# Performance work log

Measured on AMD Instinct MI355X. Metric: run time of the kernel, lower is better.

## Reference

```python
import jax, jax.numpy as jnp
import numpy as np

B, S, H, NH = 1, 4096, 1024, 16
HD = H // NH  # 64


def _rope_tables(seq_len, dim):
    inv_freq = 1.0 / (10000.0 ** (np.arange(0, dim, 2, dtype=np.float32) / dim))
    t = np.arange(seq_len, dtype=np.float32)
    freqs = np.outer(t, inv_freq)                 # [S, dim/2]
    emb = np.concatenate([freqs, freqs], axis=-1)  # [S, dim]
    return jnp.asarray(np.cos(emb)), jnp.asarray(np.sin(emb))


def setup_inputs() -> dict:
    key = jax.random.key(0)
    ks = jax.random.split(key, 5)
    hidden_states = jax.random.normal(ks[0], (B, S, H), dtype=jnp.float32)
    scale = 1.0 / np.sqrt(H)
    Wq = jax.random.normal(ks[1], (H, H), dtype=jnp.float32) * scale
    Wk = jax.random.normal(ks[2], (H, H), dtype=jnp.float32) * scale
    Wv = jax.random.normal(ks[3], (H, H), dtype=jnp.float32) * scale
    Wo = jax.random.normal(ks[4], (H, H), dtype=jnp.float32) * scale
    cos, sin = _rope_tables(S, HD)
    # additive causal mask [1,1,S,S]
    causal = jnp.where(
        jnp.tril(jnp.ones((S, S), dtype=bool)), 0.0, jnp.float32(-1e9)
    )[None, None]
    return {
        "hidden_states": hidden_states,
        "cos": cos,
        "sin": sin,
        "attention_mask": causal,
        "Wq": Wq,
        "Wk": Wk,
        "Wv": Wv,
        "Wo": Wo,
    }


def _rotate_half(x):
    x1, x2 = jnp.split(x, 2, axis=-1)
    return jnp.concatenate([-x2, x1], axis=-1)


def _apply_rope(q, k, cos, sin):
    # q,k: [B,NH,S,HD]; cos/sin: [S,HD] -> broadcast [1,1,S,HD]
    cos = cos[None, None]
    sin = sin[None, None]
    q = q * cos + _rotate_half(q) * sin
    k = k * cos + _rotate_half(k) * sin
    return q, k


def reference(hidden_states, cos, sin, attention_mask, Wq, Wk, Wv, Wo):
    bsz, q_len, _ = hidden_states.shape
    q = hidden_states @ Wq.T
    k = hidden_states @ Wk.T
    v = hidden_states @ Wv.T
    # [B,S,H] -> [B,NH,S,HD]
    def split_heads(x):
        return x.reshape(bsz, q_len, NH, HD).transpose(0, 2, 1, 3)
    q, k, v = split_heads(q), split_heads(k), split_heads(v)
    q, k = _apply_rope(q, k, cos, sin)
    scores = jnp.einsum("bhqd,bhkd->bhqk", q, k) / jnp.sqrt(jnp.float32(HD))
    scores = scores + attention_mask
    attn = jax.nn.softmax(scores, axis=-1)
    out = jnp.einsum("bhqk,bhkd->bhqd", attn, v)
    out = out.transpose(0, 2, 1, 3).reshape(bsz, q_len, H)
    return out @ Wo.T
```

## Files before the change

kernel.cpp:

```cpp
#include <hip/hip_runtime.h>

#define S_LEN 4096
#define NHEADS 16
#define HD 64
#define HDIM 1024

typedef __attribute__((ext_vector_type(8))) __bf16 bf16x8;
typedef __attribute__((ext_vector_type(4))) float f32x4;
typedef __attribute__((ext_vector_type(4))) int i32x4;
typedef unsigned short u16;

static __device__ __forceinline__ u16 f2bu(float f) {
    unsigned u = __builtin_bit_cast(unsigned, f);
    u += 0x7FFFu + ((u >> 16) & 1u);
    return (u16)(u >> 16);
}
static __device__ __forceinline__ int pack_bf16(float lo, float hi) {
    return (int)__builtin_amdgcn_perm(__builtin_bit_cast(unsigned, hi),
                                      __builtin_bit_cast(unsigned, lo), 0x07060302u);
}
static __device__ __forceinline__ float fexp2(float x) {
    return __builtin_amdgcn_exp2f(x);
}

static __device__ __forceinline__ bf16x8 read_frag(const u16* lds, int row, int kbyte) {
    int c = kbyte ^ ((row & 7) << 4);
    return *reinterpret_cast<const bf16x8*>(reinterpret_cast<const char*>(lds) + row * 128 + c);
}
static __device__ __forceinline__ bf16x8 read_off(const u16* lds, int byteoff) {
    return *reinterpret_cast<const bf16x8*>(reinterpret_cast<const char*>(lds) + byteoff);
}

static __device__ __forceinline__ void stage_gll(const u16* __restrict__ src, const u16* lds, unsigned ldsbyte) {
    __builtin_amdgcn_global_load_lds(
        (const __attribute__((address_space(1))) void*)src,
        (__attribute__((address_space(3))) void*)(reinterpret_cast<const char*>(lds) + ldsbyte),
        16, 0, 0);
}

static __device__ __forceinline__ void softmax_gather(
    const f32x4* sf, float& l_part, bf16x8* pf, int lj, int lc)
{
    int pk[4][2];
#pragma unroll
    for (int nf = 0; nf < 4; ++nf) {
        float p0 = fexp2(sf[nf][0]);
        float p1 = fexp2(sf[nf][1]);
        float p2 = fexp2(sf[nf][2]);
        float p3 = fexp2(sf[nf][3]);
        l_part += (p0 + p1) + (p2 + p3);
        pk[nf][0] = pack_bf16(p0, p1);
        pk[nf][1] = pack_bf16(p2, p3);
    }
#pragma unroll
    for (int kb = 0; kb < 2; ++kb) {
        i32x4 u;
#pragma unroll
        for (int s = 0; s < 4; ++s) {
            int srcl = lc + (((2 * lj + (s >> 1)) & 3) << 4);
            int v0 = __shfl(pk[2 * kb][s & 1], srcl);
            int v1 = __shfl(pk[2 * kb + 1][s & 1], srcl);
            u[s] = (lj & 2) ? v1 : v0;
        }
        pf[kb] = __builtin_bit_cast(bf16x8, u);
    }
}

__global__ __launch_bounds__(256) void cvt_all(
    const float* __restrict__ X, const float* __restrict__ Wq, const float* __restrict__ Wk,
    const float* __restrict__ Wv, const float* __restrict__ Wo,
    u16* __restrict__ Xb, u16* __restrict__ Wqb, u16* __restrict__ Wkb,
    u16* __restrict__ Wvb, u16* __restrict__ Wob)
{
    int i = blockIdx.x * 256 + threadIdx.x;
    const float* src; u16* dst; int off;
    if (i < (1 << 20)) { src = X; dst = Xb; off = i; }
    else {
        int j = i - (1 << 20);
        int w = j >> 18; off = j & 0x3FFFF;
        src = (w == 0) ? Wq : (w == 1) ? Wk : (w == 2) ? Wv : Wo;
        dst = (w == 0) ? Wqb : (w == 1) ? Wkb : (w == 2) ? Wvb : Wob;
    }
    float4 v = reinterpret_cast<const float4*>(src)[off];
    ushort4 o;
    o.x = f2bu(v.x); o.y = f2bu(v.y); o.z = f2bu(v.z); o.w = f2bu(v.w);
    reinterpret_cast<ushort4*>(dst)[off] = o;
}

__global__ __launch_bounds__(256) void qkv_gemm(
    const u16* __restrict__ A,
    const u16* __restrict__ Wq, const u16* __restrict__ Wk, const u16* __restrict__ Wv,
    u16* __restrict__ Qb, u16* __restrict__ Kb, u16* __restrict__ VTb,
    const float* __restrict__ cosT, const float* __restrict__ sinT)
{
    __shared__ u16 At[128 * 64];
    __shared__ u16 Bt[128 * 64];
    const int z = blockIdx.z;
    const u16* W = (z == 0) ? Wq : (z == 1) ? Wk : Wv;
    const int tid = threadIdx.x;
    const int wid = tid >> 6, lane = tid & 63;
    const int wm = wid >> 1, wn = wid & 1;
    const int lj = lane >> 4, lc = lane & 15;
    const int m0 = blockIdx.x * 128, n0 = blockIdx.y * 128;

    f32x4 acc[4][4];
#pragma unroll
    for (int i = 0; i < 4; ++i)
#pragma unroll
        for (int j = 0; j < 4; ++j) acc[i][j] = 0.0f;

    for (int k0 = 0; k0 < HDIM; k0 += 64) {
        __syncthreads();
#pragma unroll
        for (int r = 0; r < 4; ++r) {
            int idx = (r << 8) + tid;
            int row = idx >> 3;
            int c = (idx & 7) << 4;
            int csw = c ^ ((row & 7) << 4);
            unsigned lb = (unsigned)(idx & ~63) << 4;
            stage_gll(A + (size_t)(m0 + row) * HDIM + k0 + (csw >> 1), At, lb);
            stage_gll(W + (size_t)(n0 + row) * HDIM + k0 + (csw >> 1), Bt, lb);
        }
        __syncthreads();
#pragma unroll
        for (int kb = 0; kb < 2; ++kb) {
            int kbyte = (kb << 6) + (lj << 4);
            bf16x8 af[4], bfr[4];
#pragma unroll
            for (int mf = 0; mf < 4; ++mf) af[mf] = read_frag(At, (wm << 6) + (mf << 4) + lc, kbyte);
#pragma unroll
            for (int nf = 0; nf < 4; ++nf) bfr[nf] = read_frag(Bt, (wn << 6) + (nf << 4) + lc, kbyte);
#pragma unroll
            for (int mf = 0; mf < 4; ++mf)
#pragma unroll
                for (int nf = 0; nf < 4; ++nf)
                    acc[mf][nf] = __builtin_amdgcn_mfma_f32_16x16x32_bf16(af[mf], bfr[nf], acc[mf][nf], 0, 0, 0);
        }
    }

    const int mrow0 = m0 + (wm << 6);
    const int ncol0 = n0 + (wn << 6);
    if (z == 2) {
#pragma unroll
        for (int mf = 0; mf < 4; ++mf)
#pragma unroll
            for (int nf = 0; nf < 4; ++nf)
#pragma unroll
                for (int j = 0; j < 4; ++j) {
                    int s = mrow0 + (mf << 4) + (lj << 2) + j;
                    int o = ncol0 + (nf << 4) + lc;
                    VTb[((size_t)(o >> 6) * HD + (o & 63)) * S_LEN + s] = f2bu(acc[mf][nf][j]);
                }
    } else {
        u16* outB = (z == 0) ? Qb : Kb;
        const float sc = (z == 0) ? 0.18033688011112042f : 1.0f;
#pragma unroll
        for (int mf = 0; mf < 4; ++mf) {
            float nv[4][4];
#pragma unroll
            for (int nf = 0; nf < 4; ++nf)
#pragma unroll
                for (int j = 0; j < 4; ++j) {
                    int s = mrow0 + (mf << 4) + (lj << 2) + j;
                    int o = ncol0 + (nf << 4) + lc;
                    int d = o & 63;
                    float x  = acc[mf][nf][j];
                    float xp = acc[mf][nf ^ 2][j];
                    float cv = cosT[(size_t)s * HD + d];
                    float sv = sinT[(size_t)s * HD + d];
                    float rot = (d < 32) ? -xp : xp;
                    nv[nf][j] = (x * cv + rot * sv) * sc;
                }
#pragma unroll
            for (int nf = 0; nf < 4; ++nf)
#pragma unroll
                for (int j = 0; j < 4; ++j) {
                    int s = mrow0 + (mf << 4) + (lj << 2) + j;
                    int o = ncol0 + (nf << 4) + lc;
                    outB[((size_t)(o >> 6) * S_LEN + s) * HD + (o & 63)] = f2bu(nv[nf][j]);
                }
        }
    }
}

__global__ __launch_bounds__(256) void wo_gemm(
    const u16* __restrict__ A, const u16* __restrict__ W, float* __restrict__ outF)
{
    __shared__ u16 At[128 * 64];
    __shared__ u16 Bt[64 * 64];
    const int tid = threadIdx.x;
    const int wid = tid >> 6, lane = tid & 63;
    const int wm = wid >> 1, wn = wid & 1;
    const int lj = lane >> 4, lc = lane & 15;
    const int m0 = blockIdx.x * 128, n0 = blockIdx.y * 64;

    f32x4 acc[4][2];
#pragma unroll
    for (int i = 0; i < 4; ++i)
#pragma unroll
        for (int j = 0; j < 2; ++j) acc[i][j] = 0.0f;

    for (int k0 = 0; k0 < HDIM; k0 += 64) {
        __syncthreads();
#pragma unroll
        for (int r = 0; r < 4; ++r) {
            int idx = (r << 8) + tid;
            int row = idx >> 3;
            int c = (idx & 7) << 4;
            int csw = c ^ ((row & 7) << 4);
            unsigned lb = (unsigned)(idx & ~63) << 4;
            stage_gll(A + (size_t)(m0 + row) * HDIM + k0 + (csw >> 1), At, lb);
            if (r < 2)
                stage_gll(W + (size_t)(n0 + row) * HDIM + k0 + (csw >> 1), Bt, lb);
        }
        __syncthreads();
#pragma unroll
        for (int kb = 0; kb < 2; ++kb) {
            int kbyte = (kb << 6) + (lj << 4);
            bf16x8 af[4], bfr[2];
#pragma unroll
            for (int mf = 0; mf < 4; ++mf) af[mf] = read_frag(At, (wm << 6) + (mf << 4) + lc, kbyte);
#pragma unroll
            for (int nf = 0; nf < 2; ++nf) bfr[nf] = read_frag(Bt, (wn << 5) + (nf << 4) + lc, kbyte);
#pragma unroll
            for (int mf = 0; mf < 4; ++mf)
#pragma unroll
                for (int nf = 0; nf < 2; ++nf)
                    acc[mf][nf] = __builtin_amdgcn_mfma_f32_16x16x32_bf16(af[mf], bfr[nf], acc[mf][nf], 0, 0, 0);
        }
    }

    const int mrow0 = m0 + (wm << 6);
    const int ncol0 = n0 + (wn << 5);
#pragma unroll
    for (int mf = 0; mf < 4; ++mf)
#pragma unroll
        for (int nf = 0; nf < 2; ++nf)
#pragma unroll
            for (int j = 0; j < 4; ++j) {
                int s = mrow0 + (mf << 4) + (lj << 2) + j;
                int o = ncol0 + (nf << 4) + lc;
                outF[(size_t)s * HDIM + o] = acc[mf][nf][j];
            }
}

__global__ __launch_bounds__(256, 2) void attn_fwd(
    const u16* __restrict__ Q, const u16* __restrict__ K,
    const u16* __restrict__ VT, u16* __restrict__ AO)
{
    __shared__ u16 Kt[2][128 * 64];
    __shared__ u16 Vt[2][2][64 * 64];

    const int tid = threadIdx.x;
    const int wid = tid >> 6, lane = tid & 63;
    const int lj = lane >> 4, lc = lane & 15;

    const int lid = blockIdx.x;
    const int x = lid & 7, g = lid >> 3;
    const int a = g >> 5, c = g & 31;
    const int b = a ? (31 - c) : c;
    const int h = (x << 1) | a;
    const int qtA = 63 - b, qtB = b;
    const int qbaseA = qtA * 64 + wid * 16;
    const int qbaseB = qtB * 64 + wid * 16;
    const int nsteps = qtA + 1;

    const u16* Qh = Q + (size_t)h * S_LEN * HD;

    const int srow = tid >> 3;
    const int csw  = ((tid & 7) << 4) ^ ((srow & 7) << 4);
    const u16* kbase = K  + (size_t)h * S_LEN * HD + (size_t)srow * HD + (csw >> 1);
    const u16* vbase = VT + (size_t)h * HD * S_LEN + (size_t)srow * S_LEN + (csw >> 1);
    const unsigned lb = (unsigned)(tid & ~63) << 4;

#define SK(buf, hf, t) do { \
        const u16* p_ = kbase + (size_t)(t) * 64 * HD; \
        stage_gll(p_,           (const u16*)Kt[buf] + (hf) * 4096, lb); \
        stage_gll(p_ + 32 * HD, (const u16*)Kt[buf] + (hf) * 4096, lb + 4096); \
    } while (0)
#define SV(buf, hf, t) do { \
        const u16* p_ = vbase + (t) * 64; \
        stage_gll(p_,              (const u16*)Vt[buf][hf], lb); \
        stage_gll(p_ + 32 * S_LEN, (const u16*)Vt[buf][hf], lb + 4096); \
    } while (0)

    int foff[2][4];
#pragma unroll
    for (int kb = 0; kb < 2; ++kb)
#pragma unroll
        for (int nf = 0; nf < 4; ++nf) {
            int row = (nf << 4) + lc;
            foff[kb][nf] = row * 128 + (((kb << 6) + (lj << 4)) ^ ((row & 7) << 4));
        }

    bf16x8 qB0[2], qB1[2];
#pragma unroll
    for (int kb = 0; kb < 2; ++kb) {
        qB0[kb] = *reinterpret_cast<const bf16x8*>(
            Qh + (size_t)(qbaseA + lc) * HD + (kb << 5) + (lj << 3));
        qB1[kb] = *reinterpret_cast<const bf16x8*>(
            Qh + (size_t)(qbaseB + lc) * HD + (kb << 5) + (lj << 3));
    }

    f32x4 accO0[4], accO1[4];
    float l0 = 0.0f, l1 = 0.0f;
#pragma unroll
    for (int df = 0; df < 4; ++df) { accO0[df] = 0.0f; accO1[df] = 0.0f; }

    bf16x8 pf0[2], pf1[2], vf[2][4];

    auto compute = [&](int t, const u16* KtH, const u16* VtH) {
        const bool act1 = (t <= qtB);
        const bool pv1  = (t >= 1) && (t <= qtB + 1);

        bf16x8 kf[2][4];
#pragma unroll
        for (int kb = 0; kb < 2; ++kb)
#pragma unroll
            for (int nf = 0; nf < 4; ++nf)
                kf[kb][nf] = read_off(KtH, foff[kb][nf]);

        f32x4 sf0[4], sf1[4];
#pragma unroll
        for (int nf = 0; nf < 4; ++nf) { sf0[nf] = 0.0f; sf1[nf] = 0.0f; }

        __builtin_amdgcn_s_setprio(1);
#pragma unroll
        for (int kb = 0; kb < 2; ++kb)
#pragma unroll
            for (int nf = 0; nf < 4; ++nf)
                sf0[nf] = __builtin_amdgcn_mfma_f32_16x16x32_bf16(kf[kb][nf], qB0[kb], sf0[nf], 0, 0, 0);
        if (act1) {
#pragma unroll
            for (int kb = 0; kb < 2; ++kb)
#pragma unroll
                for (int nf = 0; nf < 4; ++nf)
                    sf1[nf] = __builtin_amdgcn_mfma_f32_16x16x32_bf16(kf[kb][nf], qB1[kb], sf1[nf], 0, 0, 0);
        }
        if (t >= 1) {
#pragma unroll
            for (int kb = 0; kb < 2; ++kb)
#pragma unroll
                for (int df = 0; df < 4; ++df)
                    accO0[df] = __builtin_amdgcn_mfma_f32_16x16x32_bf16(pf0[kb], vf[kb][df], accO0[df], 0, 0, 0);
        }
        if (pv1) {
#pragma unroll
            for (int kb = 0; kb < 2; ++kb)
#pragma unroll
                for (int df = 0; df < 4; ++df)
                    accO1[df] = __builtin_amdgcn_mfma_f32_16x16x32_bf16(pf1[kb], vf[kb][df], accO1[df], 0, 0, 0);
        }
        __builtin_amdgcn_s_setprio(0);

#pragma unroll
        for (int kb = 0; kb < 2; ++kb)
#pragma unroll
            for (int df = 0; df < 4; ++df)
                vf[kb][df] = read_off(VtH, foff[kb][df]);

        const int kv0 = t << 6;
        if (t == qtA) {
            int qg = qbaseA + lc;
#pragma unroll
            for (int nf = 0; nf < 4; ++nf)
#pragma unroll
                for (int j = 0; j < 4; ++j) {
                    int kvg = kv0 + (nf << 4) + (lj << 2) + j;
                    if (kvg > qg) sf0[nf][j] = -1e30f;
                }
        }
        if (act1 && t == qtB) {
            int qg = qbaseB + lc;
#pragma unroll
            for (int nf = 0; nf < 4; ++nf)
#pragma unroll
                for (int j = 0; j < 4; ++j) {
                    int kvg = kv0 + (nf << 4) + (lj << 2) + j;
                    if (kvg > qg) sf1[nf][j] = -1e30f;
                }
        }

        softmax_gather(sf0, l0, pf0, lj, lc);
        if (act1) softmax_gather(sf1, l1, pf1, lj, lc);
    };

    SK(0, 0, 0); SV(0, 0, 0);
    if (nsteps > 1) { SK(0, 1, 1); SV(0, 1, 1); }
    __syncthreads();

    const int nmac = (nsteps + 1) >> 1;
    int cur = 0;
    for (int m = 0; m < nmac; ++m) {
        const int t2 = 2 * m + 2, t3 = 2 * m + 3;
        if (t2 < nsteps) { SK(cur ^ 1, 0, t2); SV(cur ^ 1, 0, t2); }
        if (t3 < nsteps) { SK(cur ^ 1, 1, t3); SV(cur ^ 1, 1, t3); }

        compute(2 * m, (const u16*)Kt[cur], (const u16*)Vt[cur][0]);
        if (2 * m + 1 < nsteps)
            compute(2 * m + 1, (const u16*)Kt[cur] + 4096, (const u16*)Vt[cur][1]);

        __syncthreads();
        cur ^= 1;
    }

#pragma unroll
    for (int kb = 0; kb < 2; ++kb)
#pragma unroll
        for (int df = 0; df < 4; ++df)
            accO0[df] = __builtin_amdgcn_mfma_f32_16x16x32_bf16(pf0[kb], vf[kb][df], accO0[df], 0, 0, 0);

    l0 += __shfl_xor(l0, 16); l0 += __shfl_xor(l0, 32);
    l1 += __shfl_xor(l1, 16); l1 += __shfl_xor(l1, 32);
    float lr0[4], lr1[4];
#pragma unroll
    for (int j = 0; j < 4; ++j) {
        lr0[j] = __shfl(l0, (lj << 2) + j);
        lr1[j] = __shfl(l1, (lj << 2) + j);
    }
#pragma unroll
    for (int df = 0; df < 4; ++df)
#pragma unroll
        for (int j = 0; j < 4; ++j) {
            int sA = qbaseA + (lj << 2) + j;
            int sB = qbaseB + (lj << 2) + j;
            int d = (df << 4) + lc;
            AO[(size_t)sA * HDIM + h * HD + d] = f2bu(accO0[df][j] / lr0[j]);
            AO[(size_t)sB * HDIM + h * HD + d] = f2bu(accO1[df][j] / lr1[j]);
        }
#undef SK
#undef SV
}

extern "C" void kernel_launch(void* const* d_in, const int* in_sizes, int n_in,
                              void* d_out, int out_size, void* d_ws, size_t ws_size,
                              hipStream_t stream) {
    const float* hidden = (const float*)d_in[0];
    const float* cosT   = (const float*)d_in[1];
    const float* sinT   = (const float*)d_in[2];
    const float* Wq = (const float*)d_in[4];
    const float* Wk = (const float*)d_in[5];
    const float* Wv = (const float*)d_in[6];
    const float* Wo = (const float*)d_in[7];
    float* out = (float*)d_out;

    char* ws = (char*)d_ws;
    u16* Xb  = (u16*)(ws);
    u16* Wqb = (u16*)(ws + (size_t)( 8 << 20));
    u16* Wkb = (u16*)(ws + (size_t)(10 << 20));
    u16* Wvb = (u16*)(ws + (size_t)(12 << 20));
    u16* Wob = (u16*)(ws + (size_t)(14 << 20));
    u16* Qb  = (u16*)(ws + (size_t)(16 << 20));
    u16* Kb  = (u16*)(ws + (size_t)(24 << 20));
    u16* VTb = (u16*)(ws + (size_t)(32 << 20));
    u16* AOb = (u16*)(ws + (size_t)(40 << 20));

    cvt_all<<<8192, 256, 0, stream>>>(hidden, Wq, Wk, Wv, Wo, Xb, Wqb, Wkb, Wvb, Wob);

    qkv_gemm<<<dim3(S_LEN / 128, HDIM / 128, 3), 256, 0, stream>>>(
        Xb, Wqb, Wkb, Wvb, Qb, Kb, VTb, cosT, sinT);

    attn_fwd<<<dim3(512), 256, 0, stream>>>(Qb, Kb, VTb, AOb);

    wo_gemm<<<dim3(S_LEN / 128, HDIM / 64), 256, 0, stream>>>(AOb, Wob, out);
}
```

Before: 161.5 us.

## Process paired causal query tiles sequentially instead of sharing KV stream

The attention kernel previously handled two query tiles per block (a long tile and its short complement) in one pass over the KV tiles, reusing each loaded K/V tile for both. It now runs two sequential phases, one per query tile, each with its own KV pipeline. This lowers register pressure and removes the per-step branching for the second tile. In exchange, the K/V tiles for the short tile are loaded from memory a second time.

```diff
diff --git a/kernel.cpp b/kernel.cpp
--- a/kernel.cpp
+++ b/kernel.cpp
@@ -257,13 +257,8 @@
 
     const int lid = blockIdx.x;
     const int x = lid & 7, g = lid >> 3;
-    const int a = g >> 5, c = g & 31;
-    const int b = a ? (31 - c) : c;
-    const int h = (x << 1) | a;
-    const int qtA = 63 - b, qtB = b;
-    const int qbaseA = qtA * 64 + wid * 16;
-    const int qbaseB = qtB * 64 + wid * 16;
-    const int nsteps = qtA + 1;
+    const int h = (x << 1) | (g >> 5);
+    const int j = g & 31;
 
     const u16* Qh = Q + (size_t)h * S_LEN * HD;
 
@@ -293,141 +288,110 @@
             foff[kb][nf] = row * 128 + (((kb << 6) + (lj << 4)) ^ ((row & 7) << 4));
         }
 
-    bf16x8 qB0[2], qB1[2];
-#pragma unroll
-    for (int kb = 0; kb < 2; ++kb) {
-        qB0[kb] = *reinterpret_cast<const bf16x8*>(
-            Qh + (size_t)(qbaseA + lc) * HD + (kb << 5) + (lj << 3));
-        qB1[kb] = *reinterpret_cast<const bf16x8*>(
-            Qh + (size_t)(qbaseB + lc) * HD + (kb << 5) + (lj << 3));
-    }
-
-    f32x4 accO0[4], accO1[4];
-    float l0 = 0.0f, l1 = 0.0f;
-#pragma unroll
-    for (int df = 0; df < 4; ++df) { accO0[df] = 0.0f; accO1[df] = 0.0f; }
-
-    bf16x8 pf0[2], pf1[2], vf[2][4];
-
-    auto compute = [&](int t, const u16* KtH, const u16* VtH) {
-        const bool act1 = (t <= qtB);
-        const bool pv1  = (t >= 1) && (t <= qtB + 1);
-
-        bf16x8 kf[2][4];
+#pragma unroll 1
+    for (int phase = 0; phase < 2; ++phase) {
+        const int qt = phase ? j : 63 - j;
+        const int qbase = qt * 64 + wid * 16;
+        const int nsteps = qt + 1;
+
+        bf16x8 qB[2];
 #pragma unroll
         for (int kb = 0; kb < 2; ++kb)
-#pragma unroll
-            for (int nf = 0; nf < 4; ++nf)
-                kf[kb][nf] = read_off(KtH, foff[kb][nf]);
-
-        f32x4 sf0[4], sf1[4];
-#pragma unroll
-        for (int nf = 0; nf < 4; ++nf) { sf0[nf] = 0.0f; sf1[nf] = 0.0f; }
-
-        __builtin_amdgcn_s_setprio(1);
+            qB[kb] = *reinterpret_cast<const bf16x8*>(
+                Qh + (size_t)(qbase + lc) * HD + (kb << 5) + (lj << 3));
+
+        f32x4 accO[4];
+        float l0 = 0.0f;
+#pragma unroll
+        for (int df = 0; df < 4; ++df) accO[df] = 0.0f;
+
+        bf16x8 pf[2], vf[2][4];
+
+        auto compute = [&](int t, const u16* KtH, const u16* VtH) {
+            bf16x8 kf[2][4];
+#pragma unroll
+            for (int kb = 0; kb < 2; ++kb)
+#pragma unroll
+                for (int nf = 0; nf < 4; ++nf)
+                    kf[kb][nf] = read_off(KtH, foff[kb][nf]);
+
+            f32x4 sf[4];
+#pragma unroll
+            for (int nf = 0; nf < 4; ++nf) sf[nf] = 0.0f;
+
+            __builtin_amdgcn_s_setprio(1);
+#pragma unroll
+            for (int kb = 0; kb < 2; ++kb)
+#pragma unroll
+                for (int nf = 0; nf < 4; ++nf)
+                    sf[nf] = __builtin_amdgcn_mfma_f32_16x16x32_bf16(kf[kb][nf], qB[kb], sf[nf], 0, 0, 0);
+            if (t >= 1) {
+#pragma unroll
+                for (int kb = 0; kb < 2; ++kb)
+#pragma unroll
+                    for (int df = 0; df < 4; ++df)
+                        accO[df] = __builtin_amdgcn_mfma_f32_16x16x32_bf16(pf[kb], vf[kb][df], accO[df], 0, 0, 0);
+            }
+            __builtin_amdgcn_s_setprio(0);
+
+#pragma unroll
+            for (int kb = 0; kb < 2; ++kb)
+#pragma unroll
+                for (int df = 0; df < 4; ++df)
+                    vf[kb][df] = read_off(VtH, foff[kb][df]);
+
+            if (t == qt) {
+                int qg = qbase + lc;
+                int kv0 = t << 6;
+#pragma unroll
+                for (int nf = 0; nf < 4; ++nf)
+#pragma unroll
+                    for (int jj = 0; jj < 4; ++jj) {
+                        int kvg = kv0 + (nf << 4) + (lj << 2) + jj;
+                        if (kvg > qg) sf[nf][jj] = -1e30f;
+                    }
+            }
+            softmax_gather(sf, l0, pf, lj, lc);
+        };
+
+        SK(0, 0, 0); SV(0, 0, 0);
+        if (nsteps > 1) { SK(0, 1, 1); SV(0, 1, 1); }
+        __syncthreads();
+
+        const int nmac = (nsteps + 1) >> 1;
+        int cur = 0;
+        for (int m = 0; m < nmac; ++m) {
+            const int t2 = 2 * m + 2, t3 = 2 * m + 3;
+            if (t2 < nsteps) { SK(cur ^ 1, 0, t2); SV(cur ^ 1, 0, t2); }
+            if (t3 < nsteps) { SK(cur ^ 1, 1, t3); SV(cur ^ 1, 1, t3); }
+
+            compute(2 * m, (const u16*)Kt[cur], (const u16*)Vt[cur][0]);
+            if (2 * m + 1 < nsteps)
+                compute(2 * m + 1, (const u16*)Kt[cur] + 4096, (const u16*)Vt[cur][1]);
+
+            __syncthreads();
+            cur ^= 1;
+        }
+
 #pragma unroll
         for (int kb = 0; kb < 2; ++kb)
 #pragma unroll
-            for (int nf = 0; nf < 4; ++nf)
-                sf0[nf] = __builtin_amdgcn_mfma_f32_16x16x32_bf16(kf[kb][nf], qB0[kb], sf0[nf], 0, 0, 0);
-        if (act1) {
-#pragma unroll
-            for (int kb = 0; kb < 2; ++kb)
-#pragma unroll
-                for (int nf = 0; nf < 4; ++nf)
-                    sf1[nf] = __builtin_amdgcn_mfma_f32_16x16x32_bf16(kf[kb][nf], qB1[kb], sf1[nf], 0, 0, 0);
-        }
-        if (t >= 1) {
-#pragma unroll
-            for (int kb = 0; kb < 2; ++kb)
-#pragma unroll
-                for (int df = 0; df < 4; ++df)
-                    accO0[df] = __builtin_amdgcn_mfma_f32_16x16x32_bf16(pf0[kb], vf[kb][df], accO0[df], 0, 0, 0);
-        }
-        if (pv1) {
-#pragma unroll
-            for (int kb = 0; kb < 2; ++kb)
-#pragma unroll
-                for (int df = 0; df < 4; ++df)
-                    accO1[df] = __builtin_amdgcn_mfma_f32_16x16x32_bf16(pf1[kb], vf[kb][df], accO1[df], 0, 0, 0);
-        }
-        __builtin_amdgcn_s_setprio(0);
-
-#pragma unroll
-        for (int kb = 0; kb < 2; ++kb)
-#pragma unroll
             for (int df = 0; df < 4; ++df)
-                vf[kb][df] = read_off(VtH, foff[kb][df]);
-
-        const int kv0 = t << 6;
-        if (t == qtA) {
-            int qg = qbaseA + lc;
-#pragma unroll
-            for (int nf = 0; nf < 4; ++nf)
-#pragma unroll
-                for (int j = 0; j < 4; ++j) {
-                    int kvg = kv0 + (nf << 4) + (lj << 2) + j;
-                    if (kvg > qg) sf0[nf][j] = -1e30f;
-                }
-        }
-        if (act1 && t == qtB) {
-            int qg = qbaseB + lc;
-#pragma unroll
-            for (int nf = 0; nf < 4; ++nf)
-#pragma unroll
-                for (int j = 0; j < 4; ++j) {
-                    int kvg = kv0 + (nf << 4) + (lj << 2) + j;
-                    if (kvg > qg) sf1[nf][j] = -1e30f;
-                }
-        }
-
-        softmax_gather(sf0, l0, pf0, lj, lc);
-        if (act1) softmax_gather(sf1, l1, pf1, lj, lc);
-    };
-
-    SK(0, 0, 0); SV(0, 0, 0);
-    if (nsteps > 1) { SK(0, 1, 1); SV(0, 1, 1); }
-    __syncthreads();
-
-    const int nmac = (nsteps + 1) >> 1;
-    int cur = 0;
-    for (int m = 0; m < nmac; ++m) {
-        const int t2 = 2 * m + 2, t3 = 2 * m + 3;
-        if (t2 < nsteps) { SK(cur ^ 1, 0, t2); SV(cur ^ 1, 0, t2); }
-        if (t3 < nsteps) { SK(cur ^ 1, 1, t3); SV(cur ^ 1, 1, t3); }
-
-        compute(2 * m, (const u16*)Kt[cur], (const u16*)Vt[cur][0]);
-        if (2 * m + 1 < nsteps)
-            compute(2 * m + 1, (const u16*)Kt[cur] + 4096, (const u16*)Vt[cur][1]);
-
-        __syncthreads();
-        cur ^= 1;
-    }
-
-#pragma unroll
-    for (int kb = 0; kb < 2; ++kb)
+                accO[df] = __builtin_amdgcn_mfma_f32_16x16x32_bf16(pf[kb], vf[kb][df], accO[df], 0, 0, 0);
+
+        l0 += __shfl_xor(l0, 16); l0 += __shfl_xor(l0, 32);
+        float lr[4];
+#pragma unroll
+        for (int jj = 0; jj < 4; ++jj) lr[jj] = __shfl(l0, (lj << 2) + jj);
 #pragma unroll
         for (int df = 0; df < 4; ++df)
-            accO0[df] = __builtin_amdgcn_mfma_f32_16x16x32_bf16(pf0[kb], vf[kb][df], accO0[df], 0, 0, 0);
-
-    l0 += __shfl_xor(l0, 16); l0 += __shfl_xor(l0, 32);
-    l1 += __shfl_xor(l1, 16); l1 += __shfl_xor(l1, 32);
-    float lr0[4], lr1[4];
-#pragma unroll
-    for (int j = 0; j < 4; ++j) {
-        lr0[j] = __shfl(l0, (lj << 2) + j);
-        lr1[j] = __shfl(l1, (lj << 2) + j);
-    }
-#pragma unroll
-    for (int df = 0; df < 4; ++df)
-#pragma unroll
-        for (int j = 0; j < 4; ++j) {
-            int sA = qbaseA + (lj << 2) + j;
-            int sB = qbaseB + (lj << 2) + j;
-            int d = (df << 4) + lc;
-            AO[(size_t)sA * HDIM + h * HD + d] = f2bu(accO0[df][j] / lr0[j]);
-            AO[(size_t)sB * HDIM + h * HD + d] = f2bu(accO1[df][j] / lr1[j]);
-        }
+#pragma unroll
+            for (int jj = 0; jj < 4; ++jj) {
+                int s = qbase + (lj << 2) + jj;
+                int d = (df << 4) + lc;
+                AO[(size_t)s * HDIM + h * HD + d] = f2bu(accO[df][jj] / lr[jj]);
+            }
+    }
 #undef SK
 #undef SV
 }
```

Result: no change. 161.2 us (-0.2%).
